# Optimization experiments

Hardware: AMD Instinct MI355X
Metric: run time of the kernel (lower is better)

The kernel has to match this reference:

```python
import jax, jax.numpy as jnp
import numpy as np

B, S, E, H = 4, 2048, 2048, 16
HD = E // H  # 128
SCALE = 1.0 / float(np.sqrt(HD))


def setup_inputs() -> dict:
    key = jax.random.key(0)
    ks = jax.random.split(key, 9)
    std = 0.02
    return {
        "QKV": jax.random.normal(ks[0], (B, S, E), dtype=jnp.float32),
        "Wq": jax.random.normal(ks[1], (E, E), dtype=jnp.float32) * std,
        "bq": jnp.zeros((E,), dtype=jnp.float32),
        "Wk": jax.random.normal(ks[2], (E, E), dtype=jnp.float32) * std,
        "bk": jnp.zeros((E,), dtype=jnp.float32),
        "Wv": jax.random.normal(ks[3], (E, E), dtype=jnp.float32) * std,
        "bv": jnp.zeros((E,), dtype=jnp.float32),
        "Wo": jax.random.normal(ks[4], (E, E), dtype=jnp.float32) * std,
        "bo": jnp.zeros((E,), dtype=jnp.float32),
        "is_causal": 1,
    }


def _split_heads(x):
    # [B,S,E] -> [B,H,S,HD]
    return x.reshape(B, -1, H, HD).transpose(0, 2, 1, 3)


def reference(QKV, Wq, bq, Wk, bk, Wv, bv, Wo, bo, is_causal):
    # nn.Linear: y = x @ W.T + b
    Q = _split_heads(QKV @ Wq.T + bq)
    K = _split_heads(QKV @ Wk.T + bk)
    V = _split_heads(QKV @ Wv.T + bv)
    P = jnp.einsum("bhqd,bhkd->bhqk", Q, K) * SCALE
    # FAITHFUL: original masked_fill uses (ones_like(...) == 0) -> all-False
    # mask, so causal masking is a no-op regardless of is_causal.
    P = jax.nn.softmax(P, axis=-1)
    out = jnp.einsum("bhqk,bhkd->bhqd", P, V)
    out = out.transpose(0, 2, 1, 3).reshape(B, -1, E)  # [B,S,E]
    return out @ Wo.T + bo
```

## Files before the change

### kernel.cpp

```cpp
#include <hip/hip_runtime.h>
#include <stdint.h>

#define BB 4
#define SS 2048
#define EE 2048
#define HH 16
#define HD 128
#define QSCALE 0.1275174490044696f

typedef __attribute__((ext_vector_type(8))) short bf16x8;
typedef __attribute__((ext_vector_type(4))) float f32x4;

__device__ __forceinline__ unsigned short f2bf(float f) {
  union { float f; unsigned u; } v;
  v.f = f;
  unsigned r = (v.u + 0x7fffu + ((v.u >> 16) & 1u)) >> 16;
  return (unsigned short)r;
}

__device__ __forceinline__ void lds16(const void* g, void* l) {
  __builtin_amdgcn_global_load_lds(
      (__attribute__((address_space(1))) void*)(uintptr_t)g,
      (__attribute__((address_space(3))) void*)(uintptr_t)l,
      16, 0, 0);
}

__global__ void cvt_f32_bf16(const float* __restrict__ src,
                             unsigned short* __restrict__ dst, int n4) {
  int i = blockIdx.x * blockDim.x + threadIdx.x;
  if (i >= n4) return;
  float4 v = ((const float4*)src)[i];
  ushort4 o;
  o.x = f2bf(v.x); o.y = f2bf(v.y); o.z = f2bf(v.z); o.w = f2bf(v.w);
  ((ushort4*)dst)[i] = o;
}

__global__ void cvt_w3(const float* __restrict__ Wq,
                       const float* __restrict__ Wk,
                       const float* __restrict__ Wv,
                       unsigned short* __restrict__ dst, int n4each) {
  const int which = blockIdx.y;
  const float* src = (which == 0) ? Wq : (which == 1) ? Wk : Wv;
  unsigned short* d = dst + (size_t)which * 4194304;
  int i = blockIdx.x * blockDim.x + threadIdx.x;
  if (i >= n4each) return;
  float4 v = ((const float4*)src)[i];
  ushort4 o;
  o.x = f2bf(v.x); o.y = f2bf(v.y); o.z = f2bf(v.z); o.w = f2bf(v.w);
  ((ushort4*)d)[i] = o;
}

__device__ __forceinline__ void gemm256_core(
    const unsigned short* __restrict__ A,
    const unsigned short* __restrict__ Bm,
    char* lds, int m0, int n0, f32x4 acc[8][4]) {
  const int t = threadIdx.x;
  const int w = t >> 6;
  const int ln = t & 63;
  const int lr = ln & 15;
  const int lg = ln >> 4;
  const int wr = w >> 2;
  const int wc = w & 3;

  unsigned offs[4][2];
  int dof[4][2];
#pragma unroll
  for (int h = 0; h < 2; ++h)
#pragma unroll
    for (int s = 0; s < 2; ++s) {
      const int C = s * 512 + w * 64 + ln;
      const int row = C >> 3;
      const int kch = (C & 7) ^ (row & 7);
      offs[h][s]     = (unsigned)(m0 + h * 128 + row) * EE + kch * 8;
      offs[2 + h][s] = (unsigned)(n0 + h * 128 + row) * EE + kch * 8;
      dof[h][s] = h * 16384 + (s * 512 + w * 64) * 16;
      dof[2 + h][s] = 32768 + h * 16384 + (s * 512 + w * 64) * 16;
    }

#pragma unroll
  for (int i = 0; i < 8; ++i)
#pragma unroll
    for (int j = 0; j < 4; ++j) acc[i][j] = (f32x4){0.f, 0.f, 0.f, 0.f};

#pragma unroll
  for (int q = 0; q < 4; ++q)
#pragma unroll
    for (int s = 0; s < 2; ++s)
      lds16(((q < 2) ? A : Bm) + offs[q][s], lds + dof[q][s]);
  __syncthreads();

  const int cc0 = lg ^ (lr & 7);
  const int cc1 = (4 + lg) ^ (lr & 7);
  const int brbase = (wc & 1) * 64;

  bf16x8 afr[4][2];
  bf16x8 bfr[2][2][2];
  int bufo = 0;
  for (int kt = 0; kt < EE; kt += 64) {
    char* cb = lds + bufo;
    char* pb = lds + (bufo ^ 65536);
    const char* Ard = cb + wr * 16384;
    const char* Brd = cb + 32768 + (wc >> 1) * 16384;
    const bool pre = (kt + 64 < EE);
#pragma unroll
    for (int ph = 0; ph < 4; ++ph) {
      const int qm = ph >> 1, qn = ph & 1;
      if (qn == 0) {
#pragma unroll
        for (int i = 0; i < 4; ++i) {
          const int r = qm * 64 + i * 16 + lr;
          afr[i][0] = *(const bf16x8*)(Ard + r * 128 + cc0 * 16);
          afr[i][1] = *(const bf16x8*)(Ard + r * 128 + cc1 * 16);
        }
      }
      if (ph < 2) {
#pragma unroll
        for (int j = 0; j < 2; ++j) {
          const int r = brbase + ph * 32 + j * 16 + lr;
          bfr[ph][j][0] = *(const bf16x8*)(Brd + r * 128 + cc0 * 16);
          bfr[ph][j][1] = *(const bf16x8*)(Brd + r * 128 + cc1 * 16);
        }
      }
      if (pre) {
        lds16(((ph < 2) ? A : Bm) + (offs[ph][0] + (kt + 64)), pb + dof[ph][0]);
        lds16(((ph < 2) ? A : Bm) + (offs[ph][1] + (kt + 64)), pb + dof[ph][1]);
      }
      __builtin_amdgcn_s_barrier();
      __builtin_amdgcn_s_setprio(1);
#pragma unroll
      for (int i = 0; i < 4; ++i)
#pragma unroll
        for (int j = 0; j < 2; ++j) {
          acc[qm * 4 + i][qn * 2 + j] = __builtin_amdgcn_mfma_f32_16x16x32_bf16(
              afr[i][0], bfr[qn][j][0], acc[qm * 4 + i][qn * 2 + j], 0, 0, 0);
          acc[qm * 4 + i][qn * 2 + j] = __builtin_amdgcn_mfma_f32_16x16x32_bf16(
              afr[i][1], bfr[qn][j][1], acc[qm * 4 + i][qn * 2 + j], 0, 0, 0);
        }
      __builtin_amdgcn_s_setprio(0);
      if (ph < 3) {
        __builtin_amdgcn_s_barrier();
      } else {
        __syncthreads();
      }
    }
    bufo ^= 65536;
  }
}

__global__ __launch_bounds__(512, 1)
void gemm_qkv(const unsigned short* __restrict__ X,
              const unsigned short* __restrict__ W,
              const float* __restrict__ bq,
              const float* __restrict__ bk,
              const float* __restrict__ bv,
              unsigned short* __restrict__ Qb,
              unsigned short* __restrict__ Kb,
              unsigned short* __restrict__ Vb) {
  __shared__ __align__(16) char lds[131072];
  const int m0 = blockIdx.y * 256;
  const int n0 = blockIdx.x * 256;
  f32x4 acc[8][4];
  gemm256_core(X, W, lds, m0, n0, acc);

  const int t = threadIdx.x;
  const int w = t >> 6;
  const int lr = t & 15;
  const int lg = (t & 63) >> 4;
  const int wrm = (w >> 2) * 128;
  const int wcn = (w & 3) * 64;

  const int region = n0 >> 11;
  unsigned short* Dst = (region == 0) ? Qb : (region == 1) ? Kb : Vb;
  const float* bp = (region == 0) ? bq : (region == 1) ? bk : bv;

  if (region == 2) {
#pragma unroll
    for (int mi = 0; mi < 8; ++mi) {
      const int row0 = m0 + wrm + mi * 16 + lg * 4;
      const int b = row0 >> 11;
      const int s = row0 & 2047;
#pragma unroll
      for (int nj = 0; nj < 4; ++nj) {
        const int c = (n0 + wcn + nj * 16 + lr) & 2047;
        const float bias = bp[c];
        const int h = c >> 7, hd = c & 127;
        const size_t base = ((size_t)(b * HH + h) * HD + hd) * SS + s;
#pragma unroll
        for (int re = 0; re < 4; ++re)
          Dst[base + re] = f2bf(acc[mi][nj][re] + bias);
      }
    }
  } else {
    const float osc = (region == 0) ? QSCALE : 1.0f;
#pragma unroll
    for (int mi = 0; mi < 8; ++mi) {
      const int row0 = m0 + wrm + mi * 16 + lg * 4;
      const int b = row0 >> 11;
      const int s = row0 & 2047;
#pragma unroll
      for (int nj = 0; nj < 4; ++nj) {
        const int c = (n0 + wcn + nj * 16 + lr) & 2047;
        const float bias = bp[c];
        const int h = c >> 7, hd = c & 127;
        const size_t base = ((size_t)(b * HH + h) * SS + s) * HD + hd;
#pragma unroll
        for (int re = 0; re < 4; ++re)
          Dst[base + (size_t)re * HD] = f2bf((acc[mi][nj][re] + bias) * osc);
      }
    }
  }
}

__global__ __launch_bounds__(512, 1)
void gemm_out(const unsigned short* __restrict__ A,
              const unsigned short* __restrict__ W,
              const float* __restrict__ bo,
              float* __restrict__ Out) {
  __shared__ __align__(16) char lds[131072];
  const int m0 = blockIdx.y * 256;
  const int n0 = blockIdx.x * 256;
  f32x4 acc[8][4];
  gemm256_core(A, W, lds, m0, n0, acc);

  const int t = threadIdx.x;
  const int w = t >> 6;
  const int lr = t & 15;
  const int lg = (t & 63) >> 4;
  const int wrm = (w >> 2) * 128;
  const int wcn = (w & 3) * 64;

#pragma unroll
  for (int mi = 0; mi < 8; ++mi) {
    const int row0 = m0 + wrm + mi * 16 + lg * 4;
#pragma unroll
    for (int nj = 0; nj < 4; ++nj) {
      const int col = n0 + wcn + nj * 16 + lr;
      const float bias = bo[col];
#pragma unroll
      for (int re = 0; re < 4; ++re)
        Out[(size_t)(row0 + re) * EE + col] = acc[mi][nj][re] + bias;
    }
  }
}

__global__ __launch_bounds__(256, 2)
void attn_mfma(const unsigned short* __restrict__ Qb,
               const unsigned short* __restrict__ Kb,
               const unsigned short* __restrict__ Vtb,
               unsigned short* __restrict__ At) {
  __shared__ __align__(16) char lds[81920];
  const int t = threadIdx.x;
  const int w = t >> 6;
  const int ln = t & 63;
  const int lr = ln & 15;
  const int lg = ln >> 4;
  char* Ps = lds + 65536 + w * 4096;

  const int bh = blockIdx.y;
  const int qw = blockIdx.x * 128 + w * 32;

  const unsigned short* Qh = Qb + (size_t)bh * SS * HD;
  const unsigned short* Kh = Kb + (size_t)bh * SS * HD;
  const unsigned short* Vh = Vtb + (size_t)bh * HD * SS;

  bf16x8 qfr[2][4];
#pragma unroll
  for (int qi = 0; qi < 2; ++qi)
#pragma unroll
    for (int ds = 0; ds < 4; ++ds)
      qfr[qi][ds] = *(const bf16x8*)(Qh + (size_t)(qw + qi * 16 + lr) * HD + ds * 32 + lg * 8);

  f32x4 acc[8][2];
#pragma unroll
  for (int df = 0; df < 8; ++df)
#pragma unroll
    for (int qi = 0; qi < 2; ++qi)
      acc[df][qi] = (f32x4){0.f, 0.f, 0.f, 0.f};
  float mrun[2] = {-3.0e38f, -3.0e38f};
  float lsum[2] = {0.f, 0.f};

#define STAGE_KV(kt, buf)                                                      \
  do {                                                                         \
    char* Kd = lds + (buf) * 32768;                                            \
    char* Vd = Kd + 16384;                                                     \
    _Pragma("unroll") for (int i = 0; i < 4; ++i) {                            \
      const int c = i * 256 + w * 64 + ln;                                     \
      const int row = c >> 4;                                                  \
      const int gch = (c & 15) ^ (row & 7);                                    \
      lds16(Kh + (size_t)((kt) + row) * HD + gch * 8,                          \
            Kd + (i * 256 + w * 64) * 16);                                     \
    }                                                                          \
    _Pragma("unroll") for (int i = 0; i < 4; ++i) {                            \
      const int c = i * 256 + w * 64 + ln;                                     \
      const int d = c >> 3;                                                    \
      const int kc = (c & 7) ^ (d & 7);                                        \
      lds16(Vh + (size_t)d * SS + (kt) + kc * 8,                               \
            Vd + (i * 256 + w * 64) * 16);                                     \
    }                                                                          \
  } while (0)

  STAGE_KV(0, 0);
  __syncthreads();

  int cur = 0;
  for (int kt = 0; kt < SS; kt += 64) {
    if (kt + 64 < SS) STAGE_KV(kt + 64, cur ^ 1);

    char* Ks = lds + cur * 32768;
    char* Vs = Ks + 16384;

    f32x4 st[4][2];
    __builtin_amdgcn_s_setprio(1);
#pragma unroll
    for (int kf = 0; kf < 4; ++kf) {
#pragma unroll
      for (int qi = 0; qi < 2; ++qi) st[kf][qi] = (f32x4){0.f, 0.f, 0.f, 0.f};
#pragma unroll
      for (int ds = 0; ds < 4; ++ds) {
        const int krow = kf * 16 + lr;
        bf16x8 kfr = *(const bf16x8*)(Ks + krow * 256 + (((ds * 4 + lg) ^ (krow & 7)) * 16));
#pragma unroll
        for (int qi = 0; qi < 2; ++qi)
          st[kf][qi] = __builtin_amdgcn_mfma_f32_16x16x32_bf16(kfr, qfr[qi][ds], st[kf][qi], 0, 0, 0);
      }
    }
    __builtin_amdgcn_s_setprio(0);

#pragma unroll
    for (int qi = 0; qi < 2; ++qi) {
      float tm = st[0][qi][0];
#pragma unroll
      for (int kf = 0; kf < 4; ++kf)
#pragma unroll
        for (int r = 0; r < 4; ++r) tm = fmaxf(tm, st[kf][qi][r]);
      tm = fmaxf(tm, __shfl_xor(tm, 16, 64));
      tm = fmaxf(tm, __shfl_xor(tm, 32, 64));
      if (!__all(tm <= mrun[qi] + 8.0f)) {
        const float mnew = fmaxf(mrun[qi], tm);
        const float alpha = __builtin_exp2f(mrun[qi] - mnew);
        mrun[qi] = mnew;
        lsum[qi] *= alpha;
#pragma unroll
        for (int df = 0; df < 8; ++df) {
          acc[df][qi][0] *= alpha; acc[df][qi][1] *= alpha;
          acc[df][qi][2] *= alpha; acc[df][qi][3] *= alpha;
        }
      }
      const float mcur = mrun[qi];
      float rs = 0.f;
      const int qrow = qi * 16 + lr;
#pragma unroll
      for (int kf = 0; kf < 4; ++kf) {
        const float p0 = __builtin_exp2f(st[kf][qi][0] - mcur);
        const float p1 = __builtin_exp2f(st[kf][qi][1] - mcur);
        const float p2 = __builtin_exp2f(st[kf][qi][2] - mcur);
        const float p3 = __builtin_exp2f(st[kf][qi][3] - mcur);
        rs += (p0 + p1) + (p2 + p3);
        ushort4 pk;
        pk.x = f2bf(p0); pk.y = f2bf(p1); pk.z = f2bf(p2); pk.w = f2bf(p3);
        const int k0 = kf * 16 + lg * 4;
        *(ushort4*)(Ps + qrow * 128 + (((k0 >> 3) ^ (qrow & 7)) * 16) + (k0 & 7) * 2) = pk;
      }
      lsum[qi] += rs;
    }

    bf16x8 pf[2][2];
#pragma unroll
    for (int ks = 0; ks < 2; ++ks)
#pragma unroll
      for (int qi = 0; qi < 2; ++qi) {
        const int qrow = qi * 16 + lr;
        pf[ks][qi] = *(const bf16x8*)(Ps + qrow * 128 + (((ks * 4 + lg) ^ (qrow & 7)) * 16));
      }
    __builtin_amdgcn_s_setprio(1);
#pragma unroll
    for (int df = 0; df < 8; ++df) {
#pragma unroll
      for (int ks = 0; ks < 2; ++ks) {
        const int drow = df * 16 + lr;
        bf16x8 vfr = *(const bf16x8*)(Vs + drow * 128 + (((ks * 4 + lg) ^ (drow & 7)) * 16));
#pragma unroll
        for (int qi = 0; qi < 2; ++qi)
          acc[df][qi] = __builtin_amdgcn_mfma_f32_16x16x32_bf16(vfr, pf[ks][qi], acc[df][qi], 0, 0, 0);
      }
    }
    __builtin_amdgcn_s_setprio(0);

    __syncthreads();
    cur ^= 1;
  }

  const int b = bh >> 4, h = bh & 15;
#pragma unroll
  for (int qi = 0; qi < 2; ++qi) {
    float l = lsum[qi];
    l += __shfl_xor(l, 16, 64);
    l += __shfl_xor(l, 32, 64);
    const float rl = 1.0f / l;
    const int s = qw + qi * 16 + lr;
    unsigned short* orow = At + ((size_t)(b * SS + s)) * EE + h * HD;
#pragma unroll
    for (int df = 0; df < 8; ++df)
#pragma unroll
      for (int r = 0; r < 4; ++r)
        orow[df * 16 + lg * 4 + r] = f2bf(acc[df][qi][r] * rl);
  }
}

extern "C" void kernel_launch(void* const* d_in, const int* in_sizes, int n_in,
                              void* d_out, int out_size, void* d_ws, size_t ws_size,
                              hipStream_t stream) {
  const float* QKV = (const float*)d_in[0];
  const float* Wq  = (const float*)d_in[1];
  const float* bq  = (const float*)d_in[2];
  const float* Wk  = (const float*)d_in[3];
  const float* bk  = (const float*)d_in[4];
  const float* Wv  = (const float*)d_in[5];
  const float* bv  = (const float*)d_in[6];
  const float* Wo  = (const float*)d_in[7];
  const float* bo  = (const float*)d_in[8];

  unsigned short* Xb = (unsigned short*)d_out;

  char* ws = (char*)d_ws;
  unsigned short* Wqkvb = (unsigned short*)(ws);
  unsigned short* Qb    = (unsigned short*)(ws + ( 24u << 20));
  unsigned short* Kb    = (unsigned short*)(ws + ( 56u << 20));
  unsigned short* Vb    = (unsigned short*)(ws + ( 88u << 20));
  unsigned short* At    = (unsigned short*)(ws + (120u << 20));
  unsigned short* Wob   = Wqkvb;

  cvt_f32_bf16<<<dim3(16384), dim3(256), 0, stream>>>(QKV, Xb, 4194304);
  cvt_w3<<<dim3(4096, 3), dim3(256), 0, stream>>>(Wq, Wk, Wv, Wqkvb, 1048576);

  gemm_qkv<<<dim3(24, 32), dim3(512), 0, stream>>>(Xb, Wqkvb, bq, bk, bv, Qb, Kb, Vb);
  attn_mfma<<<dim3(16, 64), dim3(256), 0, stream>>>(Qb, Kb, Vb, At);

  cvt_f32_bf16<<<dim3(4096), dim3(256), 0, stream>>>(Wo, Wob, 1048576);
  gemm_out<<<dim3(8, 32), dim3(512), 0, stream>>>(At, Wob, bo, (float*)d_out);
}
```

Before: 614.3 us.

## Transpose softmax P tile in registers via lane shuffles instead of LDS round-trip

The attention kernel no longer writes the bf16 probability tile to a per-wave LDS scratch area and reads it back as MFMA B-operand fragments. It packs the values with v_cvt_pk_bf16_f32 and rearranges them across lanes with two rounds of xor shuffles, which shrinks LDS from 80 KB to 64 KB and could allow more blocks per CU. K/V staging addresses are now precomputed and advanced by pointer increments instead of being recomputed each tile. In exchange the lanes do extra shuffle and select work, and the shuffle permutation must exactly reproduce the old fragment layout.

```diff
diff --git a/kernel.cpp b/kernel.cpp
--- a/kernel.cpp
+++ b/kernel.cpp
@@ -248,13 +248,17 @@
                const unsigned short* __restrict__ Kb,
                const unsigned short* __restrict__ Vtb,
                unsigned short* __restrict__ At) {
-  __shared__ __align__(16) char lds[81920];
+  __shared__ __align__(16) char lds[65536];
   const int t = threadIdx.x;
   const int w = t >> 6;
   const int ln = t & 63;
   const int lr = ln & 15;
   const int lg = ln >> 4;
-  char* Ps = lds + 65536 + w * 4096;
+  const int la = lg >> 1;
+  const int lb = lg & 1;
+  const bool sela = (la == 0);
+  const bool abeq = (la == lb);
+  const bool b0eq = (lb == 0);
 
   const int bh = blockIdx.y;
   const int qw = blockIdx.x * 128 + w * 32;
@@ -279,32 +283,40 @@
   float mrun[2] = {-3.0e38f, -3.0e38f};
   float lsum[2] = {0.f, 0.f};
 
-#define STAGE_KV(kt, buf)                                                      \
+  const unsigned short* gk[4];
+  const unsigned short* gv[4];
+  int ldk[4], ldv[4];
+#pragma unroll
+  for (int i = 0; i < 4; ++i) {
+    const int c = i * 256 + w * 64 + ln;
+    const int row = c >> 4;
+    const int gch = (c & 15) ^ (row & 7);
+    gk[i] = Kh + (size_t)row * HD + gch * 8;
+    const int d = c >> 3;
+    const int kc = (c & 7) ^ (d & 7);
+    gv[i] = Vh + (size_t)d * SS + kc * 8;
+    ldk[i] = (i * 256 + w * 64) * 16;
+    ldv[i] = 16384 + (i * 256 + w * 64) * 16;
+  }
+
+#define STAGE_KV(bufbase)                                                      \
   do {                                                                         \
-    char* Kd = lds + (buf) * 32768;                                            \
-    char* Vd = Kd + 16384;                                                     \
     _Pragma("unroll") for (int i = 0; i < 4; ++i) {                            \
-      const int c = i * 256 + w * 64 + ln;                                     \
-      const int row = c >> 4;                                                  \
-      const int gch = (c & 15) ^ (row & 7);                                    \
-      lds16(Kh + (size_t)((kt) + row) * HD + gch * 8,                          \
-            Kd + (i * 256 + w * 64) * 16);                                     \
+      lds16(gk[i], (bufbase) + ldk[i]);                                        \
+      lds16(gv[i], (bufbase) + ldv[i]);                                        \
     }                                                                          \
     _Pragma("unroll") for (int i = 0; i < 4; ++i) {                            \
-      const int c = i * 256 + w * 64 + ln;                                     \
-      const int d = c >> 3;                                                    \
-      const int kc = (c & 7) ^ (d & 7);                                        \
-      lds16(Vh + (size_t)d * SS + (kt) + kc * 8,                               \
-            Vd + (i * 256 + w * 64) * 16);                                     \
+      gk[i] += 64 * HD;                                                        \
+      gv[i] += 64;                                                             \
     }                                                                          \
   } while (0)
 
-  STAGE_KV(0, 0);
+  STAGE_KV(lds);
   __syncthreads();
 
   int cur = 0;
   for (int kt = 0; kt < SS; kt += 64) {
-    if (kt + 64 < SS) STAGE_KV(kt + 64, cur ^ 1);
+    if (kt + 64 < SS) STAGE_KV(lds + ((cur ^ 1) * 32768));
 
     char* Ks = lds + cur * 32768;
     char* Vs = Ks + 16384;
@@ -326,6 +338,7 @@
     }
     __builtin_amdgcn_s_setprio(0);
 
+    bf16x8 pf[2][2];
 #pragma unroll
     for (int qi = 0; qi < 2; ++qi) {
       float tm = st[0][qi][0];
@@ -348,7 +361,7 @@
       }
       const float mcur = mrun[qi];
       float rs = 0.f;
-      const int qrow = qi * 16 + lr;
+      unsigned cell[4][2];
 #pragma unroll
       for (int kf = 0; kf < 4; ++kf) {
         const float p0 = __builtin_exp2f(st[kf][qi][0] - mcur);
@@ -356,22 +369,40 @@
         const float p2 = __builtin_exp2f(st[kf][qi][2] - mcur);
         const float p3 = __builtin_exp2f(st[kf][qi][3] - mcur);
         rs += (p0 + p1) + (p2 + p3);
-        ushort4 pk;
-        pk.x = f2bf(p0); pk.y = f2bf(p1); pk.z = f2bf(p2); pk.w = f2bf(p3);
-        const int k0 = kf * 16 + lg * 4;
-        *(ushort4*)(Ps + qrow * 128 + (((k0 >> 3) ^ (qrow & 7)) * 16) + (k0 & 7) * 2) = pk;
+        asm("v_cvt_pk_bf16_f32 %0, %1, %2" : "=v"(cell[kf][0]) : "v"(p0), "v"(p1));
+        asm("v_cvt_pk_bf16_f32 %0, %1, %2" : "=v"(cell[kf][1]) : "v"(p2), "v"(p3));
       }
       lsum[qi] += rs;
-    }
-
-    bf16x8 pf[2][2];
-#pragma unroll
-    for (int ks = 0; ks < 2; ++ks)
-#pragma unroll
-      for (int qi = 0; qi < 2; ++qi) {
-        const int qrow = qi * 16 + lr;
-        pf[ks][qi] = *(const bf16x8*)(Ps + qrow * 128 + (((ks * 4 + lg) ^ (qrow & 7)) * 16));
-      }
+
+      unsigned own1[2][2], rcv1[2][2];
+#pragma unroll
+      for (int j = 0; j < 2; ++j)
+#pragma unroll
+        for (int i = 0; i < 2; ++i) {
+          const unsigned snd = sela ? cell[2 * j + 1][i] : cell[2 * j][i];
+          rcv1[j][i] = (unsigned)__shfl_xor((int)snd, 32, 64);
+          own1[j][i] = sela ? cell[2 * j][i] : cell[2 * j + 1][i];
+        }
+      unsigned kp[2][2], rr[2][2];
+#pragma unroll
+      for (int j = 0; j < 2; ++j)
+#pragma unroll
+        for (int i = 0; i < 2; ++i) {
+          const unsigned s2 = abeq ? rcv1[j][i] : own1[j][i];
+          rr[j][i] = (unsigned)__shfl_xor((int)s2, 16, 64);
+          kp[j][i] = abeq ? own1[j][i] : rcv1[j][i];
+        }
+#pragma unroll
+      for (int ks = 0; ks < 2; ++ks) {
+        union { unsigned u[4]; bf16x8 v; } pk;
+        pk.u[0] = b0eq ? kp[ks][0] : rr[ks][0];
+        pk.u[1] = b0eq ? kp[ks][1] : rr[ks][1];
+        pk.u[2] = b0eq ? rr[ks][0] : kp[ks][0];
+        pk.u[3] = b0eq ? rr[ks][1] : kp[ks][1];
+        pf[ks][qi] = pk.v;
+      }
+    }
+
     __builtin_amdgcn_s_setprio(1);
 #pragma unroll
     for (int df = 0; df < 8; ++df) {
```

Result: no change. 611.7 us (-0.4%).
